# Kernel optimization log

Hardware: AMD Instinct MI355X
Metric: run time of the kernel (lower is better)

The kernel has to match this reference:

```python
import jax, jax.numpy as jnp
import numpy as np

HEAD_SIZE = 64

def setup_inputs() -> dict:
    key = jax.random.key(0)
    k1, k2, k3, k4 = jax.random.split(key, 4)
    B, T, D = 4, 4096, 768
    x = jax.random.normal(k1, (B, T, D), dtype=jnp.float32)
    Wq = jax.random.normal(k2, (D, HEAD_SIZE), dtype=jnp.float32) * (1.0 / np.sqrt(D))
    Wk = jax.random.normal(k3, (D, HEAD_SIZE), dtype=jnp.float32) * (1.0 / np.sqrt(D))
    Wv = jax.random.normal(k4, (D, HEAD_SIZE), dtype=jnp.float32) * (1.0 / np.sqrt(D))
    return {"x": x, "Wq": Wq, "Wk": Wk, "Wv": Wv}

def reference(x, Wq, Wk, Wv):
    # q,k,v: [B, T, H]
    q = jnp.einsum('btd,dh->bth', x, Wq)
    k = jnp.einsum('btd,dh->bth', x, Wk)
    v = jnp.einsum('btd,dh->bth', x, Wv)
    # scores: [B, T, T]; causal mask via lower-triangular band, -inf elsewhere
    scores = jnp.einsum('bqh,bkh->bqk', q, k)
    T = x.shape[1]
    causal = jnp.tril(jnp.ones((T, T), dtype=bool))  # band_part(ones, -1, 0)
    scores = jnp.where(causal[None, :, :], scores, -jnp.inf)
    attn = jax.nn.softmax(scores / np.sqrt(HEAD_SIZE), axis=-1)
    # dropout is identity in eval mode
    return jnp.einsum('bqk,bkh->bqh', attn, v)
```

## Files before the change

### kernel.cpp

```cpp
#include <hip/hip_runtime.h>
#include <math.h>

typedef __attribute__((ext_vector_type(8))) short short8;
typedef __attribute__((ext_vector_type(4))) float f32x4;
typedef unsigned short ushort_t;

#define TSEQ   4096
#define NBATCH 4
#define DMODEL 768
#define HS     64
#define KSPLIT 4

static __device__ __forceinline__ ushort_t f2bf(float f) {
  union { float f; unsigned u; } v; v.f = f;
  unsigned r = v.u + 0x7fffu + ((v.u >> 16) & 1u);
  return (ushort_t)(r >> 16);
}
static __device__ __forceinline__ float bf2f(ushort_t u) {
  union { unsigned u; float f; } v; v.u = ((unsigned)u) << 16; return v.f;
}

#define MFMA16(a,b,c) __builtin_amdgcn_mfma_f32_16x16x32_bf16((a),(b),(c),0,0,0)

__global__ __launch_bounds__(256) void wprep(
    const float* __restrict__ Wq, const float* __restrict__ Wk,
    const float* __restrict__ Wv, ushort_t* __restrict__ Wt)
{
  __shared__ float lds[64 * 65];
  const int m = blockIdx.x / 12, kc = blockIdx.x % 12, k0 = kc * 64;
  const float* W = (m == 0) ? Wq : (m == 1) ? Wk : Wv;
  const int tid = threadIdx.x;
#pragma unroll
  for (int i = 0; i < 16; i++) {
    const int row = i * 4 + (tid >> 6), col = tid & 63;
    lds[row * 65 + col] = W[(size_t)(k0 + row) * HS + col];
  }
  __syncthreads();
#pragma unroll
  for (int i = 0; i < 16; i++) {
    const int n = i * 4 + (tid >> 6), kk = tid & 63;
    Wt[(size_t)(m * 64 + n) * DMODEL + k0 + kk] = f2bf(lds[kk * 65 + n]);
  }
}

__global__ __launch_bounds__(256, 2) void qkv_mfma(
    const float* __restrict__ x, const ushort_t* __restrict__ Wt,
    ushort_t* __restrict__ q, ushort_t* __restrict__ kO, ushort_t* __restrict__ vT)
{
  __shared__ __align__(16) ushort_t Abuf[2][32 * 72];

  const int tid  = threadIdx.x;
  const int w    = tid >> 6, lane = tid & 63;
  const int l16  = lane & 15, quad = lane >> 4;
  const int mh   = w >> 1, ns = w & 1;
  const int M0   = blockIdx.x * 32;
  const float* xg = x + (size_t)M0 * DMODEL;

  const int srow = tid >> 3, scol = (tid & 7) * 8;
  const float* xs = xg + (size_t)srow * DMODEL + scol;
  const ushort_t* wb = Wt + (size_t)(ns * 96 + l16) * DMODEL + quad * 8;

  f32x4 acc[6];
#pragma unroll
  for (int nt = 0; nt < 6; nt++) acc[nt] = (f32x4){0.f, 0.f, 0.f, 0.f};

  float4 pr0 = *(const float4*)(xs);
  float4 pr1 = *(const float4*)(xs + 4);
  short8 bpre[12];
#pragma unroll
  for (int nt = 0; nt < 6; nt++)
#pragma unroll
    for (int kc = 0; kc < 2; kc++)
      bpre[nt * 2 + kc] = *(const short8*)(wb + (size_t)nt * 16 * DMODEL + kc * 32);

  for (int ks = 0; ks < DMODEL / 64; ks++) {
    ushort_t* Ab = &Abuf[ks & 1][0];
    {
      short8 p;
      p[0]=f2bf(pr0.x); p[1]=f2bf(pr0.y); p[2]=f2bf(pr0.z); p[3]=f2bf(pr0.w);
      p[4]=f2bf(pr1.x); p[5]=f2bf(pr1.y); p[6]=f2bf(pr1.z); p[7]=f2bf(pr1.w);
      *(short8*)(Ab + srow * 72 + scol) = p;
    }
    if (ks < DMODEL / 64 - 1) {
      const float* xn = xs + (ks + 1) * 64;
      pr0 = *(const float4*)(xn);
      pr1 = *(const float4*)(xn + 4);
    }
    __syncthreads();
    short8 bcur[12];
#pragma unroll
    for (int t = 0; t < 12; t++) bcur[t] = bpre[t];
    if (ks < DMODEL / 64 - 1) {
#pragma unroll
      for (int nt = 0; nt < 6; nt++)
#pragma unroll
        for (int kc = 0; kc < 2; kc++)
          bpre[nt * 2 + kc] =
              *(const short8*)(wb + (size_t)nt * 16 * DMODEL + (ks + 1) * 64 + kc * 32);
    }
#pragma unroll
    for (int kc = 0; kc < 2; kc++) {
      const short8 af = *(const short8*)(Ab + (mh * 16 + l16) * 72 + kc * 32 + quad * 8);
#pragma unroll
      for (int nt = 0; nt < 6; nt++) acc[nt] = MFMA16(af, bcur[nt * 2 + kc], acc[nt]);
    }
  }

#pragma unroll
  for (int nt = 0; nt < 6; nt++) {
    const int gnt = ns * 6 + nt;
    const int mat = gnt >> 2;
    if (mat <= 1) {
      const int col = (gnt & 3) * 16 + l16;
#pragma unroll
      for (int r = 0; r < 4; r++) {
        const float val = acc[nt][r];
        const int trow = M0 + mh * 16 + quad * 4 + r;
        if (mat == 0) q [(size_t)trow * HS + col] = f2bf(val * 0.125f);
        else          kO[(size_t)trow * HS + col] = f2bf(val);
      }
    }
  }
  __syncthreads();
  float* vls = (float*)&Abuf[0][0];
  if (ns == 1) {
#pragma unroll
    for (int nt = 2; nt < 6; nt++) {
      const int vcol = ((ns * 6 + nt) & 3) * 16 + l16;
#pragma unroll
      for (int r = 0; r < 4; r++)
        vls[(mh * 16 + quad * 4 + r) * 65 + vcol] = acc[nt][r];
    }
  }
  __syncthreads();
  const int d = tid >> 2, seg = tid & 3;
  short8 pk;
#pragma unroll
  for (int i = 0; i < 8; i++) pk[i] = (short)f2bf(vls[(seg * 8 + i) * 65 + d]);
  *(short8*)(vT + ((size_t)(M0 >> 12) * HS + d) * TSEQ + (M0 & (TSEQ - 1)) + seg * 8) = pk;
}

#define KP 72
__global__ __launch_bounds__(128) void attn_part(
    const ushort_t* __restrict__ q, const ushort_t* __restrict__ k,
    const ushort_t* __restrict__ vT, float* __restrict__ ML, ushort_t* __restrict__ OP)
{
  __shared__ __align__(16) ushort_t sK[64 * KP];
  __shared__ __align__(16) ushort_t sV[64 * KP];
  __shared__ __align__(16) ushort_t sP[2][16 * KP];

  const int idx  = blockIdx.x;
  const int s    = idx & 3;
  const int b    = (idx >> 2) & 3;
  const int jt   = 127 - (idx >> 4);
  const int tid  = threadIdx.x;
  const int w    = tid >> 6;
  const int lane = tid & 63;
  const int l16  = lane & 15, quad = lane >> 4;
  const int R0   = jt * 32 + w * 16;

  const ushort_t* qg = q  + (size_t)b * TSEQ * HS;
  const ushort_t* kg = k  + (size_t)b * TSEQ * HS;
  const ushort_t* vg = vT + (size_t)b * HS * TSEQ;

  const short8 qf0 = *(const short8*)(qg + (R0 + l16) * HS +      quad * 8);
  const short8 qf1 = *(const short8*)(qg + (R0 + l16) * HS + 32 + quad * 8);

  f32x4 o[4];
#pragma unroll
  for (int dt = 0; dt < 4; dt++) o[dt] = (f32x4){0.f, 0.f, 0.f, 0.f};
  float mrow = -INFINITY, lrow = 0.f;

  const int nkt = jt / 2 + 1;
  short8 kpre[4], vpre[4];
  int kt = s;
  if (kt < nkt) {
    const int k0 = kt * 64;
#pragma unroll
    for (int i = 0; i < 4; i++) {
      const int c = i * 128 + tid, key = c >> 3, ch = c & 7;
      kpre[i] = *(const short8*)(kg + (size_t)(k0 + key) * HS + ch * 8);
      vpre[i] = *(const short8*)(vg + (size_t)key * TSEQ + k0 + ch * 8);
    }
  }
  for (; kt < nkt; kt += KSPLIT) {
    const int k0 = kt * 64;
    __syncthreads();
#pragma unroll
    for (int i = 0; i < 4; i++) {
      const int c = i * 128 + tid, key = c >> 3, ch = c & 7;
      *(short8*)(sK + key * KP + ch * 8) = kpre[i];
      *(short8*)(sV + key * KP + ch * 8) = vpre[i];
    }
    if (kt + KSPLIT < nkt) {
      const int kn = (kt + KSPLIT) * 64;
#pragma unroll
      for (int i = 0; i < 4; i++) {
        const int c = i * 128 + tid, key = c >> 3, ch = c & 7;
        kpre[i] = *(const short8*)(kg + (size_t)(kn + key) * HS + ch * 8);
        vpre[i] = *(const short8*)(vg + (size_t)key * TSEQ + kn + ch * 8);
      }
    }
    __syncthreads();
    f32x4 sT[4];
#pragma unroll
    for (int ct = 0; ct < 4; ct++) {
      sT[ct] = (f32x4){0.f, 0.f, 0.f, 0.f};
      const short8 kfa = *(const short8*)(sK + (ct * 16 + l16) * KP +      quad * 8);
      const short8 kfb = *(const short8*)(sK + (ct * 16 + l16) * KP + 32 + quad * 8);
      sT[ct] = MFMA16(kfa, qf0, sT[ct]);
      sT[ct] = MFMA16(kfb, qf1, sT[ct]);
    }
    if (k0 + 63 > R0) {
      const int qrow = R0 + l16;
#pragma unroll
      for (int ct = 0; ct < 4; ct++)
#pragma unroll
        for (int r = 0; r < 4; r++)
          sT[ct][r] = (k0 + ct * 16 + quad * 4 + r <= qrow) ? sT[ct][r] : -INFINITY;
    }
    float tm = -INFINITY;
#pragma unroll
    for (int ct = 0; ct < 4; ct++)
#pragma unroll
      for (int r = 0; r < 4; r++) tm = fmaxf(tm, sT[ct][r]);
    tm = fmaxf(tm, __shfl_xor(tm, 16));
    tm = fmaxf(tm, __shfl_xor(tm, 32));
    const float mn = fmaxf(mrow, tm);
    const float al = __expf(mrow - mn);
    mrow = mn;
    float ps = 0.f;
#pragma unroll
    for (int ct = 0; ct < 4; ct++)
#pragma unroll
      for (int r = 0; r < 4; r++) { sT[ct][r] = __expf(sT[ct][r] - mn); ps += sT[ct][r]; }
    ps += __shfl_xor(ps, 16);
    ps += __shfl_xor(ps, 32);
    lrow = lrow * al + ps;
    ushort_t* Pw = &sP[w][0];
#pragma unroll
    for (int ct = 0; ct < 4; ct++) {
      ushort4 pk;
      pk.x = f2bf(sT[ct][0]); pk.y = f2bf(sT[ct][1]);
      pk.z = f2bf(sT[ct][2]); pk.w = f2bf(sT[ct][3]);
      *(ushort4*)(Pw + l16 * KP + ct * 16 + quad * 4) = pk;
    }
    float alo[4];
#pragma unroll
    for (int r = 0; r < 4; r++) alo[r] = __shfl(al, quad * 4 + r);
#pragma unroll
    for (int dt = 0; dt < 4; dt++)
#pragma unroll
      for (int r = 0; r < 4; r++) o[dt][r] *= alo[r];
    const short8 pf0 = *(const short8*)(Pw + l16 * KP +      quad * 8);
    const short8 pf1 = *(const short8*)(Pw + l16 * KP + 32 + quad * 8);
#pragma unroll
    for (int dt = 0; dt < 4; dt++) {
      const short8 vfa = *(const short8*)(sV + (dt * 16 + l16) * KP +      quad * 8);
      const short8 vfb = *(const short8*)(sV + (dt * 16 + l16) * KP + 32 + quad * 8);
      o[dt] = MFMA16(pf0, vfa, o[dt]);
      o[dt] = MFMA16(pf1, vfb, o[dt]);
    }
  }

  const size_t base = ((size_t)(b * KSPLIT + s) * TSEQ);
  if (quad == 0) {
    ML[(base + R0 + l16) * 2 + 0] = mrow;
    ML[(base + R0 + l16) * 2 + 1] = lrow;
  }
#pragma unroll
  for (int dt = 0; dt < 4; dt++)
#pragma unroll
    for (int r = 0; r < 4; r++)
      OP[(base + R0 + quad * 4 + r) * HS + dt * 16 + l16] = f2bf(o[dt][r]);
}

__global__ __launch_bounds__(256) void attn_merge(
    const float* __restrict__ ML, const ushort_t* __restrict__ OP,
    float* __restrict__ out)
{
  const int row = blockIdx.x * 16 + (threadIdx.x >> 4);
  const int b   = row >> 12, t = row & (TSEQ - 1);
  const int d0  = (threadIdx.x & 15) * 4;
  float m[KSPLIT], l[KSPLIT];
  float M = -INFINITY;
#pragma unroll
  for (int ss = 0; ss < KSPLIT; ss++) {
    const size_t i = ((size_t)(b * KSPLIT + ss) * TSEQ + t);
    m[ss] = ML[i * 2]; l[ss] = ML[i * 2 + 1];
    M = fmaxf(M, m[ss]);
  }
  float den = 0.f;
  float4 num = make_float4(0.f, 0.f, 0.f, 0.f);
#pragma unroll
  for (int ss = 0; ss < KSPLIT; ss++) {
    const float a = __expf(m[ss] - M);
    den += l[ss] * a;
    const size_t i = ((size_t)(b * KSPLIT + ss) * TSEQ + t);
    const ushort4 u = *(const ushort4*)(OP + i * HS + d0);
    num.x += a * bf2f(u.x); num.y += a * bf2f(u.y);
    num.z += a * bf2f(u.z); num.w += a * bf2f(u.w);
  }
  const float inv = 1.f / den;
  *(float4*)(out + (size_t)row * HS + d0) =
      make_float4(num.x * inv, num.y * inv, num.z * inv, num.w * inv);
}

extern "C" void kernel_launch(void* const* d_in, const int* in_sizes, int n_in,
                              void* d_out, int out_size, void* d_ws, size_t ws_size,
                              hipStream_t stream) {
  const float* x  = (const float*)d_in[0];
  const float* Wq = (const float*)d_in[1];
  const float* Wk = (const float*)d_in[2];
  const float* Wv = (const float*)d_in[3];
  float* out = (float*)d_out;

  char* ws = (char*)d_ws;
  ushort_t* Wt = (ushort_t*)ws;
  ushort_t* qb = (ushort_t*)(ws + 294912);
  ushort_t* kb = (ushort_t*)(ws + 294912 + 2097152);
  ushort_t* vb = (ushort_t*)(ws + 294912 + 2 * 2097152);
  float*    ml = (float*)   (ws + 294912 + 3 * 2097152);
  ushort_t* op = (ushort_t*)(ws + 294912 + 3 * 2097152 + 524288);

  wprep<<<36, 256, 0, stream>>>(Wq, Wk, Wv, Wt);
  qkv_mfma<<<(NBATCH * TSEQ) / 32, 256, 0, stream>>>(x, Wt, qb, kb, vb);
  attn_part<<<128 * NBATCH * KSPLIT, 128, 0, stream>>>(qb, kb, vb, ml, op);
  attn_merge<<<1024, 256, 0, stream>>>(ml, op, out);
}
```

Before: 148.7 us.

## Drop LDS staging in QKV projection and overlap K/V prefetch with attention compute

The QKV projection kernel no longer stages x through shared memory with block barriers. Each wave now loads its own 16-row A fragments straight from global memory, keeping a four-deep register pipeline of A and B chunks, and only V goes through a small per-wave LDS transpose. The grid becomes 512 blocks of 4 independent waves. In attn_part, loading the next K/V tile is moved so the global loads are issued before the current tile's MFMA/softmax work and written to LDS after it, to hide load latency. In exchange, register pressure rises and each wave re-reads x directly from global memory.

```diff
diff --git a/kernel.cpp b/kernel.cpp
--- a/kernel.cpp
+++ b/kernel.cpp
@@ -47,97 +47,79 @@
     const float* __restrict__ x, const ushort_t* __restrict__ Wt,
     ushort_t* __restrict__ q, ushort_t* __restrict__ kO, ushort_t* __restrict__ vT)
 {
-  __shared__ __align__(16) ushort_t Abuf[2][32 * 72];
+  __shared__ __align__(16) float vls[4][16 * 68];
 
   const int tid  = threadIdx.x;
   const int w    = tid >> 6, lane = tid & 63;
   const int l16  = lane & 15, quad = lane >> 4;
-  const int mh   = w >> 1, ns = w & 1;
-  const int M0   = blockIdx.x * 32;
-  const float* xg = x + (size_t)M0 * DMODEL;
-
-  const int srow = tid >> 3, scol = (tid & 7) * 8;
-  const float* xs = xg + (size_t)srow * DMODEL + scol;
-  const ushort_t* wb = Wt + (size_t)(ns * 96 + l16) * DMODEL + quad * 8;
+  const int gw   = blockIdx.x * 4 + w;
+  const int R0   = (gw >> 1) * 16;
+  const int nHalf = gw & 1;
+
+  const float* xr = x + (size_t)(R0 + l16) * DMODEL + quad * 8;
+  const ushort_t* wb = Wt + (size_t)(nHalf * 96 + l16) * DMODEL + quad * 8;
 
   f32x4 acc[6];
 #pragma unroll
   for (int nt = 0; nt < 6; nt++) acc[nt] = (f32x4){0.f, 0.f, 0.f, 0.f};
 
-  float4 pr0 = *(const float4*)(xs);
-  float4 pr1 = *(const float4*)(xs + 4);
-  short8 bpre[12];
-#pragma unroll
-  for (int nt = 0; nt < 6; nt++)
-#pragma unroll
-    for (int kc = 0; kc < 2; kc++)
-      bpre[nt * 2 + kc] = *(const short8*)(wb + (size_t)nt * 16 * DMODEL + kc * 32);
-
-  for (int ks = 0; ks < DMODEL / 64; ks++) {
-    ushort_t* Ab = &Abuf[ks & 1][0];
-    {
-      short8 p;
-      p[0]=f2bf(pr0.x); p[1]=f2bf(pr0.y); p[2]=f2bf(pr0.z); p[3]=f2bf(pr0.w);
-      p[4]=f2bf(pr1.x); p[5]=f2bf(pr1.y); p[6]=f2bf(pr1.z); p[7]=f2bf(pr1.w);
-      *(short8*)(Ab + srow * 72 + scol) = p;
+  float4 ar[4][2];
+  short8 br[4][6];
+#pragma unroll
+  for (int j = 0; j < 4; j++) {
+    ar[j][0] = *(const float4*)(xr + j * 32);
+    ar[j][1] = *(const float4*)(xr + j * 32 + 4);
+#pragma unroll
+    for (int nt = 0; nt < 6; nt++)
+      br[j][nt] = *(const short8*)(wb + (size_t)nt * 16 * DMODEL + j * 32);
+  }
+
+  for (int mi = 0; mi < 6; mi++) {
+#pragma unroll
+    for (int j = 0; j < 4; j++) {
+      short8 af;
+      af[0]=f2bf(ar[j][0].x); af[1]=f2bf(ar[j][0].y);
+      af[2]=f2bf(ar[j][0].z); af[3]=f2bf(ar[j][0].w);
+      af[4]=f2bf(ar[j][1].x); af[5]=f2bf(ar[j][1].y);
+      af[6]=f2bf(ar[j][1].z); af[7]=f2bf(ar[j][1].w);
+#pragma unroll
+      for (int nt = 0; nt < 6; nt++) acc[nt] = MFMA16(af, br[j][nt], acc[nt]);
+      const int kn = mi * 4 + j + 4;
+      if (kn < 24) {
+        ar[j][0] = *(const float4*)(xr + kn * 32);
+        ar[j][1] = *(const float4*)(xr + kn * 32 + 4);
+#pragma unroll
+        for (int nt = 0; nt < 6; nt++)
+          br[j][nt] = *(const short8*)(wb + (size_t)nt * 16 * DMODEL + kn * 32);
+      }
     }
-    if (ks < DMODEL / 64 - 1) {
-      const float* xn = xs + (ks + 1) * 64;
-      pr0 = *(const float4*)(xn);
-      pr1 = *(const float4*)(xn + 4);
+  }
+
+#pragma unroll
+  for (int nt = 0; nt < 6; nt++) {
+    const int gnt = nHalf * 6 + nt;
+    const int mat = gnt >> 2;
+    const int col = (gnt & 3) * 16 + l16;
+#pragma unroll
+    for (int r = 0; r < 4; r++) {
+      const float val = acc[nt][r];
+      const int trow = R0 + quad * 4 + r;
+      if (mat == 0)      q [(size_t)trow * HS + col] = f2bf(val * 0.125f);
+      else if (mat == 1) kO[(size_t)trow * HS + col] = f2bf(val);
+      else               vls[w][(quad * 4 + r) * 68 + col] = val;
     }
-    __syncthreads();
-    short8 bcur[12];
-#pragma unroll
-    for (int t = 0; t < 12; t++) bcur[t] = bpre[t];
-    if (ks < DMODEL / 64 - 1) {
-#pragma unroll
-      for (int nt = 0; nt < 6; nt++)
-#pragma unroll
-        for (int kc = 0; kc < 2; kc++)
-          bpre[nt * 2 + kc] =
-              *(const short8*)(wb + (size_t)nt * 16 * DMODEL + (ks + 1) * 64 + kc * 32);
-    }
-#pragma unroll
-    for (int kc = 0; kc < 2; kc++) {
-      const short8 af = *(const short8*)(Ab + (mh * 16 + l16) * 72 + kc * 32 + quad * 8);
-#pragma unroll
-      for (int nt = 0; nt < 6; nt++) acc[nt] = MFMA16(af, bcur[nt * 2 + kc], acc[nt]);
-    }
-  }
-
-#pragma unroll
-  for (int nt = 0; nt < 6; nt++) {
-    const int gnt = ns * 6 + nt;
-    const int mat = gnt >> 2;
-    if (mat <= 1) {
-      const int col = (gnt & 3) * 16 + l16;
-#pragma unroll
-      for (int r = 0; r < 4; r++) {
-        const float val = acc[nt][r];
-        const int trow = M0 + mh * 16 + quad * 4 + r;
-        if (mat == 0) q [(size_t)trow * HS + col] = f2bf(val * 0.125f);
-        else          kO[(size_t)trow * HS + col] = f2bf(val);
-      }
-    }
-  }
-  __syncthreads();
-  float* vls = (float*)&Abuf[0][0];
-  if (ns == 1) {
-#pragma unroll
-    for (int nt = 2; nt < 6; nt++) {
-      const int vcol = ((ns * 6 + nt) & 3) * 16 + l16;
-#pragma unroll
-      for (int r = 0; r < 4; r++)
-        vls[(mh * 16 + quad * 4 + r) * 65 + vcol] = acc[nt][r];
-    }
-  }
-  __syncthreads();
-  const int d = tid >> 2, seg = tid & 3;
-  short8 pk;
-#pragma unroll
-  for (int i = 0; i < 8; i++) pk[i] = (short)f2bf(vls[(seg * 8 + i) * 65 + d]);
-  *(short8*)(vT + ((size_t)(M0 >> 12) * HS + d) * TSEQ + (M0 & (TSEQ - 1)) + seg * 8) = pk;
+  }
+  if (nHalf == 1) {
+    const int d = lane;
+    short8 p0, p1;
+#pragma unroll
+    for (int i = 0; i < 8; i++) p0[i] = (short)f2bf(vls[w][i * 68 + d]);
+#pragma unroll
+    for (int i = 0; i < 8; i++) p1[i] = (short)f2bf(vls[w][(8 + i) * 68 + d]);
+    ushort_t* dst = vT + ((size_t)(R0 >> 12) * HS + d) * TSEQ + (R0 & (TSEQ - 1));
+    *(short8*)(dst)     = p0;
+    *(short8*)(dst + 8) = p1;
+  }
 }
 
 #define KP 72
@@ -172,94 +154,106 @@
   float mrow = -INFINITY, lrow = 0.f;
 
   const int nkt = jt / 2 + 1;
-  short8 kpre[4], vpre[4];
-  int kt = s;
-  if (kt < nkt) {
-    const int k0 = kt * 64;
-#pragma unroll
-    for (int i = 0; i < 4; i++) {
-      const int c = i * 128 + tid, key = c >> 3, ch = c & 7;
-      kpre[i] = *(const short8*)(kg + (size_t)(k0 + key) * HS + ch * 8);
-      vpre[i] = *(const short8*)(vg + (size_t)key * TSEQ + k0 + ch * 8);
-    }
-  }
-  for (; kt < nkt; kt += KSPLIT) {
-    const int k0 = kt * 64;
-    __syncthreads();
-#pragma unroll
-    for (int i = 0; i < 4; i++) {
-      const int c = i * 128 + tid, key = c >> 3, ch = c & 7;
-      *(short8*)(sK + key * KP + ch * 8) = kpre[i];
-      *(short8*)(sV + key * KP + ch * 8) = vpre[i];
-    }
-    if (kt + KSPLIT < nkt) {
-      const int kn = (kt + KSPLIT) * 64;
+  if (s < nkt) {
+    {
+      const int k0 = s * 64;
+      short8 kpre[4], vpre[4];
 #pragma unroll
       for (int i = 0; i < 4; i++) {
         const int c = i * 128 + tid, key = c >> 3, ch = c & 7;
-        kpre[i] = *(const short8*)(kg + (size_t)(kn + key) * HS + ch * 8);
-        vpre[i] = *(const short8*)(vg + (size_t)key * TSEQ + kn + ch * 8);
-      }
+        kpre[i] = *(const short8*)(kg + (size_t)(k0 + key) * HS + ch * 8);
+        vpre[i] = *(const short8*)(vg + (size_t)key * TSEQ + k0 + ch * 8);
+      }
+#pragma unroll
+      for (int i = 0; i < 4; i++) {
+        const int c = i * 128 + tid, key = c >> 3, ch = c & 7;
+        *(short8*)(sK + key * KP + ch * 8) = kpre[i];
+        *(short8*)(sV + key * KP + ch * 8) = vpre[i];
+      }
+      __syncthreads();
     }
-    __syncthreads();
-    f32x4 sT[4];
-#pragma unroll
-    for (int ct = 0; ct < 4; ct++) {
-      sT[ct] = (f32x4){0.f, 0.f, 0.f, 0.f};
-      const short8 kfa = *(const short8*)(sK + (ct * 16 + l16) * KP +      quad * 8);
-      const short8 kfb = *(const short8*)(sK + (ct * 16 + l16) * KP + 32 + quad * 8);
-      sT[ct] = MFMA16(kfa, qf0, sT[ct]);
-      sT[ct] = MFMA16(kfb, qf1, sT[ct]);
-    }
-    if (k0 + 63 > R0) {
-      const int qrow = R0 + l16;
+    for (int kt = s; kt < nkt; kt += KSPLIT) {
+      const int k0 = kt * 64;
+      const int kn = kt + KSPLIT;
+      short8 kpre[4], vpre[4];
+      if (kn < nkt) {
+        const int g0 = kn * 64;
+#pragma unroll
+        for (int i = 0; i < 4; i++) {
+          const int c = i * 128 + tid, key = c >> 3, ch = c & 7;
+          kpre[i] = *(const short8*)(kg + (size_t)(g0 + key) * HS + ch * 8);
+          vpre[i] = *(const short8*)(vg + (size_t)key * TSEQ + g0 + ch * 8);
+        }
+      }
+      f32x4 sT[4];
+#pragma unroll
+      for (int ct = 0; ct < 4; ct++) {
+        sT[ct] = (f32x4){0.f, 0.f, 0.f, 0.f};
+        const short8 kfa = *(const short8*)(sK + (ct * 16 + l16) * KP +      quad * 8);
+        const short8 kfb = *(const short8*)(sK + (ct * 16 + l16) * KP + 32 + quad * 8);
+        sT[ct] = MFMA16(kfa, qf0, sT[ct]);
+        sT[ct] = MFMA16(kfb, qf1, sT[ct]);
+      }
+      if (k0 + 63 > R0) {
+        const int qrow = R0 + l16;
+#pragma unroll
+        for (int ct = 0; ct < 4; ct++)
+#pragma unroll
+          for (int r = 0; r < 4; r++)
+            sT[ct][r] = (k0 + ct * 16 + quad * 4 + r <= qrow) ? sT[ct][r] : -INFINITY;
+      }
+      float tm = -INFINITY;
 #pragma unroll
       for (int ct = 0; ct < 4; ct++)
 #pragma unroll
-        for (int r = 0; r < 4; r++)
-          sT[ct][r] = (k0 + ct * 16 + quad * 4 + r <= qrow) ? sT[ct][r] : -INFINITY;
-    }
-    float tm = -INFINITY;
-#pragma unroll
-    for (int ct = 0; ct < 4; ct++)
-#pragma unroll
-      for (int r = 0; r < 4; r++) tm = fmaxf(tm, sT[ct][r]);
-    tm = fmaxf(tm, __shfl_xor(tm, 16));
-    tm = fmaxf(tm, __shfl_xor(tm, 32));
-    const float mn = fmaxf(mrow, tm);
-    const float al = __expf(mrow - mn);
-    mrow = mn;
-    float ps = 0.f;
-#pragma unroll
-    for (int ct = 0; ct < 4; ct++)
-#pragma unroll
-      for (int r = 0; r < 4; r++) { sT[ct][r] = __expf(sT[ct][r] - mn); ps += sT[ct][r]; }
-    ps += __shfl_xor(ps, 16);
-    ps += __shfl_xor(ps, 32);
-    lrow = lrow * al + ps;
-    ushort_t* Pw = &sP[w][0];
-#pragma unroll
-    for (int ct = 0; ct < 4; ct++) {
-      ushort4 pk;
-      pk.x = f2bf(sT[ct][0]); pk.y = f2bf(sT[ct][1]);
-      pk.z = f2bf(sT[ct][2]); pk.w = f2bf(sT[ct][3]);
-      *(ushort4*)(Pw + l16 * KP + ct * 16 + quad * 4) = pk;
-    }
-    float alo[4];
-#pragma unroll
-    for (int r = 0; r < 4; r++) alo[r] = __shfl(al, quad * 4 + r);
-#pragma unroll
-    for (int dt = 0; dt < 4; dt++)
-#pragma unroll
-      for (int r = 0; r < 4; r++) o[dt][r] *= alo[r];
-    const short8 pf0 = *(const short8*)(Pw + l16 * KP +      quad * 8);
-    const short8 pf1 = *(const short8*)(Pw + l16 * KP + 32 + quad * 8);
-#pragma unroll
-    for (int dt = 0; dt < 4; dt++) {
-      const short8 vfa = *(const short8*)(sV + (dt * 16 + l16) * KP +      quad * 8);
-      const short8 vfb = *(const short8*)(sV + (dt * 16 + l16) * KP + 32 + quad * 8);
-      o[dt] = MFMA16(pf0, vfa, o[dt]);
-      o[dt] = MFMA16(pf1, vfb, o[dt]);
+        for (int r = 0; r < 4; r++) tm = fmaxf(tm, sT[ct][r]);
+      tm = fmaxf(tm, __shfl_xor(tm, 16));
+      tm = fmaxf(tm, __shfl_xor(tm, 32));
+      const float mn = fmaxf(mrow, tm);
+      const float al = __expf(mrow - mn);
+      mrow = mn;
+      float ps = 0.f;
+#pragma unroll
+      for (int ct = 0; ct < 4; ct++)
+#pragma unroll
+        for (int r = 0; r < 4; r++) { sT[ct][r] = __expf(sT[ct][r] - mn); ps += sT[ct][r]; }
+      ps += __shfl_xor(ps, 16);
+      ps += __shfl_xor(ps, 32);
+      lrow = lrow * al + ps;
+      ushort_t* Pw = &sP[w][0];
+#pragma unroll
+      for (int ct = 0; ct < 4; ct++) {
+        ushort4 pk;
+        pk.x = f2bf(sT[ct][0]); pk.y = f2bf(sT[ct][1]);
+        pk.z = f2bf(sT[ct][2]); pk.w = f2bf(sT[ct][3]);
+        *(ushort4*)(Pw + l16 * KP + ct * 16 + quad * 4) = pk;
+      }
+      float alo[4];
+#pragma unroll
+      for (int r = 0; r < 4; r++) alo[r] = __shfl(al, quad * 4 + r);
+#pragma unroll
+      for (int dt = 0; dt < 4; dt++)
+#pragma unroll
+        for (int r = 0; r < 4; r++) o[dt][r] *= alo[r];
+      const short8 pf0 = *(const short8*)(Pw + l16 * KP +      quad * 8);
+      const short8 pf1 = *(const short8*)(Pw + l16 * KP + 32 + quad * 8);
+#pragma unroll
+      for (int dt = 0; dt < 4; dt++) {
+        const short8 vfa = *(const short8*)(sV + (dt * 16 + l16) * KP +      quad * 8);
+        const short8 vfb = *(const short8*)(sV + (dt * 16 + l16) * KP + 32 + quad * 8);
+        o[dt] = MFMA16(pf0, vfa, o[dt]);
+        o[dt] = MFMA16(pf1, vfb, o[dt]);
+      }
+      if (kn < nkt) {
+        __syncthreads();
+#pragma unroll
+        for (int i = 0; i < 4; i++) {
+          const int c = i * 128 + tid, key = c >> 3, ch = c & 7;
+          *(short8*)(sK + key * KP + ch * 8) = kpre[i];
+          *(short8*)(sV + key * KP + ch * 8) = vpre[i];
+        }
+        __syncthreads();
+      }
     }
   }
 
@@ -324,7 +318,7 @@
   ushort_t* op = (ushort_t*)(ws + 294912 + 3 * 2097152 + 524288);
 
   wprep<<<36, 256, 0, stream>>>(Wq, Wk, Wv, Wt);
-  qkv_mfma<<<(NBATCH * TSEQ) / 32, 256, 0, stream>>>(x, Wt, qb, kb, vb);
+  qkv_mfma<<<512, 256, 0, stream>>>(x, Wt, qb, kb, vb);
   attn_part<<<128 * NBATCH * KSPLIT, 128, 0, stream>>>(qb, kb, vb, ml, op);
   attn_merge<<<1024, 256, 0, stream>>>(ml, op, out);
 }
```

After: 161.3 us. +8.5%, slower.
